# Kernel optimization log

Hardware: AMD Instinct MI355X
Metric: run time of the kernel (lower is better)

Reference implementation:

```python
import jax, jax.numpy as jnp
import numpy as np
from jax import lax

DIM = 1024
EXPAND = 2
D_STATE = 16
D_CONV = 4
DT_RANK = 64  # ceil(DIM/16)
DIM_INNER = DIM * EXPAND
B_SZ, SEQ = 2, 1024


def setup_inputs() -> dict:
    key = jax.random.key(0)
    ks = jax.random.split(key, 8)
    s = lambda fan_in: 1.0 / np.sqrt(fan_in)
    x = jax.random.normal(ks[0], (B_SZ, SEQ, DIM), dtype=jnp.float32)
    W_in = jax.random.normal(ks[1], (DIM, 2 * DIM_INNER), dtype=jnp.float32) * s(DIM)
    conv_w = jax.random.normal(ks[2], (DIM_INNER, D_CONV), dtype=jnp.float32) * s(D_CONV)
    conv_b = jax.random.normal(ks[3], (DIM_INNER,), dtype=jnp.float32) * s(D_CONV)
    W_x = jax.random.normal(ks[4], (DIM_INNER, DT_RANK + 2 * D_STATE), dtype=jnp.float32) * s(DIM_INNER)
    W_dt = jax.random.normal(ks[5], (DT_RANK, DIM_INNER), dtype=jnp.float32) * s(DT_RANK)
    b_dt = jax.random.normal(ks[6], (DIM_INNER,), dtype=jnp.float32) * s(DT_RANK)
    # A_log = log(repeat(arange(1, d_state+1), 'n -> d n'))
    A_log = jnp.broadcast_to(jnp.log(jnp.arange(1, D_STATE + 1, dtype=jnp.float32)), (DIM_INNER, D_STATE))
    D = jnp.ones((DIM_INNER,), dtype=jnp.float32)
    W_out = jax.random.normal(ks[7], (DIM_INNER, DIM), dtype=jnp.float32) * s(DIM_INNER)
    return {"x": x, "W_in": W_in, "conv_w": conv_w, "conv_b": conv_b,
            "W_x": W_x, "W_dt": W_dt, "b_dt": b_dt, "A_log": A_log, "D": D, "W_out": W_out}


def _mamba_forward(x, W_in, conv_w, conv_b, W_x, W_dt, b_dt, A_log, D, W_out):
    b, l, d = x.shape
    di = W_out.shape[0]  # dim_inner
    n = A_log.shape[1]   # d_state
    dt_rank = W_dt.shape[0]

    # in_proj (no bias) and split into ssm branch / gate residual
    x_and_res = x @ W_in                      # [b, l, 2*di]
    u, res = jnp.split(x_and_res, 2, axis=-1)  # each [b, l, di]

    # causal depthwise conv1d along sequence (torch pads both sides then slices [:l])
    pad = conv_w.shape[1] - 1
    up = jnp.pad(u, ((0, 0), (pad, 0), (0, 0)))
    kernel = conv_w.T[:, None, :]  # [W=d_conv, I=1, O=di]
    u = lax.conv_general_dilated(up, kernel, window_strides=(1,), padding='VALID',
                                 dimension_numbers=('NWC', 'WIO', 'NWC'),
                                 feature_group_count=di) + conv_b
    u = jax.nn.silu(u)  # [b, l, di]

    # input-dependent SSM params
    x_dbl = u @ W_x  # [b, l, dt_rank + 2n]
    delta_r, Bm, Cm = jnp.split(x_dbl, [dt_rank, dt_rank + n], axis=-1)
    delta = jax.nn.softplus(delta_r @ W_dt + b_dt)  # [b, l, di]
    A = -jnp.exp(A_log)  # [di, n]

    deltaA = jnp.exp(jnp.einsum('bld,dn->bldn', delta, A))        # [b, l, di, n]
    deltaB_u = jnp.einsum('bld,bln,bld->bldn', delta, Bm, u)       # [b, l, di, n]

    def step(h, inp):
        dA_t, dBu_t, c_t = inp            # [b,di,n], [b,di,n], [b,n]
        h = dA_t * h + dBu_t
        y_t = jnp.einsum('bdn,bn->bd', h, c_t)
        return h, y_t

    h0 = jnp.zeros((b, di, n), dtype=u.dtype)
    xs = (jnp.moveaxis(deltaA, 1, 0), jnp.moveaxis(deltaB_u, 1, 0), jnp.moveaxis(Cm, 1, 0))
    _, ys = lax.scan(step, h0, xs)        # ys: [l, b, di]
    y = jnp.moveaxis(ys, 0, 1)            # [b, l, di]
    y = y + u * D                          # skip term

    y = y * jax.nn.silu(res)               # gate
    return y @ W_out                       # [b, l, dim]


def reference(x, W_in, conv_w, conv_b, W_x, W_dt, b_dt, A_log, D, W_out):
    return _mamba_forward(x, W_in, conv_w, conv_b, W_x, W_dt, b_dt, A_log, D, W_out)
```

## Files before the change

kernel.cpp:

```cpp
#include <hip/hip_runtime.h>
#include <hip/hip_bf16.h>
#include <math.h>


__device__ __forceinline__ float silu_f(float x) {
    return x / (1.f + __expf(-x));
}
__device__ __forceinline__ unsigned short f2bf(float f) {
    __hip_bfloat16 h = __float2bfloat16(f);
    return *(unsigned short*)&h;
}
__device__ __forceinline__ float bf2f(unsigned short u) {
    return __uint_as_float((unsigned)u << 16);
}

typedef __attribute__((ext_vector_type(8))) short short8v;
typedef __attribute__((ext_vector_type(4))) float f32x4;

__device__ __forceinline__ void gload16(const void* g, void* lds) {
    __builtin_amdgcn_global_load_lds(
        (const __attribute__((address_space(1))) unsigned int*)g,
        (__attribute__((address_space(3))) unsigned int*)lds, 16, 0, 0);
}

template<int MODE>
__global__ __launch_bounds__(256) void gemm_bf16(
    const unsigned short* __restrict__ A,
    const unsigned short* __restrict__ BT,
    float* __restrict__ C,
    unsigned short* __restrict__ Cb,
    const float* __restrict__ bias,
    int M, int N, int K, int klen)
{
    __shared__ unsigned short As[128 * 32];
    __shared__ unsigned short Bs[128 * 32];
    const int tid  = threadIdx.x;
    const int wid  = tid >> 6;
    const int lane = tid & 63;
    const int wr = wid >> 1, wc = wid & 1;
    const int row0 = blockIdx.y * 128, col0 = blockIdx.x * 128;
    const int kbeg = blockIdx.z * klen;
    C += (size_t)blockIdx.z * M * N;

    f32x4 acc[4][4] = {};

    const int srow = lane >> 2;
    const int scol = (lane & 3) * 8;

    for (int k0 = kbeg; k0 < kbeg + klen; k0 += 32) {
        #pragma unroll
        for (int c = 0; c < 2; ++c) {
            int chunk = wid * 2 + c;
            gload16(A  + (size_t)(row0 + chunk * 16 + srow) * K + k0 + scol,
                    (void*)(As + chunk * 512));
            gload16(BT + (size_t)(col0 + chunk * 16 + srow) * K + k0 + scol,
                    (void*)(Bs + chunk * 512));
        }
        __syncthreads();
        short8v a[4], b[4];
        #pragma unroll
        for (int i = 0; i < 4; ++i)
            a[i] = *(const short8v*)&As[(wr * 64 + i * 16 + (lane & 15)) * 32 + (lane >> 4) * 8];
        #pragma unroll
        for (int j = 0; j < 4; ++j)
            b[j] = *(const short8v*)&Bs[(wc * 64 + j * 16 + (lane & 15)) * 32 + (lane >> 4) * 8];
        #pragma unroll
        for (int i = 0; i < 4; ++i)
            #pragma unroll
            for (int j = 0; j < 4; ++j)
                acc[i][j] = __builtin_amdgcn_mfma_f32_16x16x32_bf16(a[i], b[j], acc[i][j], 0, 0, 0);
        __syncthreads();
    }

    #pragma unroll
    for (int i = 0; i < 4; ++i) {
        int rbase = row0 + wr * 64 + i * 16 + (lane >> 4) * 4;
        #pragma unroll
        for (int j = 0; j < 4; ++j) {
            int cc = col0 + wc * 64 + j * 16 + (lane & 15);
            float bi = (MODE == 3) ? bias[cc] : 0.f;
            #pragma unroll
            for (int r = 0; r < 4; ++r) {
                float v = acc[i][j][r];
                if (MODE == 3) {
                    v += bi;
                    v = (v > 20.f) ? v : __logf(1.f + __expf(v));
                    Cb[(size_t)(rbase + r) * N + cc] = f2bf(v);
                } else {
                    C[(size_t)(rbase + r) * N + cc] = v;
                }
            }
        }
    }
}

__device__ __forceinline__ void trans64(
    const float* __restrict__ W, unsigned short* __restrict__ WT,
    int K, int N, int bk, int bn, int tid, float (*t)[65])
{
    const int tx = tid & 63, ty = tid >> 6;
    #pragma unroll
    for (int s = 0; s < 16; ++s)
        t[ty + 4 * s][tx] = W[(size_t)(bk + ty + 4 * s) * N + bn + tx];
    __syncthreads();
    #pragma unroll
    for (int s = 0; s < 16; ++s)
        WT[(size_t)(bn + ty + 4 * s) * K + bk + tx] = f2bf(t[tx][ty + 4 * s]);
}

__global__ __launch_bounds__(256) void prep_all(
    const float* __restrict__ x,
    const float* __restrict__ W_in,
    const float* __restrict__ W_out,
    const float* __restrict__ Wx,
    const float* __restrict__ Wdt,
    unsigned short* __restrict__ xb,
    unsigned short* __restrict__ W_inT,
    unsigned short* __restrict__ W_outT,
    unsigned short* __restrict__ W_xTp,
    unsigned short* __restrict__ W_dtTp)
{
    __shared__ float t[64][65];
    const int bid = blockIdx.x;
    const int tid = threadIdx.x;
    if (bid < 1024) {
        int i = bid * 256 + tid;
        float4 v0 = *(const float4*)(x + (size_t)i * 8);
        float4 v1 = *(const float4*)(x + (size_t)i * 8 + 4);
        ushort4 o0, o1;
        o0.x = f2bf(v0.x); o0.y = f2bf(v0.y); o0.z = f2bf(v0.z); o0.w = f2bf(v0.w);
        o1.x = f2bf(v1.x); o1.y = f2bf(v1.y); o1.z = f2bf(v1.z); o1.w = f2bf(v1.w);
        *(ushort4*)(xb + (size_t)i * 8) = o0;
        *(ushort4*)(xb + (size_t)i * 8 + 4) = o1;
    } else if (bid < 2048) {
        int tt = bid - 1024;
        trans64(W_in, W_inT, 1024, 4096, (tt >> 6) * 64, (tt & 63) * 64, tid, t);
    } else if (bid < 2560) {
        int tt = bid - 2048;
        trans64(W_out, W_outT, 2048, 1024, (tt >> 4) * 64, (tt & 15) * 64, tid, t);
    } else if (bid < 3584) {
        int idx = (bid - 2560) * 256 + tid;
        int k = idx & 2047, n = idx >> 11;
        float v = (n < 96) ? Wx[(size_t)k * 96 + n] : 0.f;
        W_xTp[idx] = f2bf(v);
    } else {
        int idx = (bid - 3584) * 256 + tid;
        int k = idx & 127, n = idx >> 7;
        float v = (k < 64) ? Wdt[(size_t)k * 2048 + n] : 0.f;
        W_dtTp[idx] = f2bf(v);
    }
}

__global__ __launch_bounds__(256) void reduce16(
    const float* __restrict__ P, float* __restrict__ dst,
    unsigned short* __restrict__ dstb)
{
    int i = blockIdx.x * 256 + threadIdx.x;
    const float4* P4 = (const float4*)P;
    float4 s = P4[i];
    #pragma unroll
    for (int k = 1; k < 16; ++k) {
        float4 v = P4[i + (size_t)k * 65536];
        s.x += v.x; s.y += v.y; s.z += v.z; s.w += v.w;
    }
    ((float4*)dst)[i] = s;
    ushort4 o;
    o.x = f2bf(s.x); o.y = f2bf(s.y); o.z = f2bf(s.z); o.w = f2bf(s.w);
    ((ushort4*)dstb)[i] = o;
}

__global__ __launch_bounds__(256) void reduce2(
    const float* __restrict__ P, float* __restrict__ dst)
{
    int i = blockIdx.x * 256 + threadIdx.x;
    const float4* P4 = (const float4*)P;
    float4 a = P4[i], b = P4[i + 524288];
    a.x += b.x; a.y += b.y; a.z += b.z; a.w += b.w;
    ((float4*)dst)[i] = a;
}

__global__ __launch_bounds__(256) void conv_silu(
    const float* __restrict__ xr,
    const float* __restrict__ conv_w,
    const float* __restrict__ conv_b,
    unsigned short* __restrict__ ub)
{
    int idx = blockIdx.x * 256 + threadIdx.x;
    int d = idx & 2047;
    int r = idx >> 11;
    int l = r & 1023;
    int b = r >> 10;
    float acc = conv_b[d];
    const float* wp = conv_w + d * 4;
    #pragma unroll
    for (int w = 0; w < 4; ++w) {
        int ls = l + w - 3;
        if (ls >= 0)
            acc = fmaf(xr[((size_t)((b << 10) + ls) << 12) + d], wp[w], acc);
    }
    ub[idx] = f2bf(silu_f(acc));
}

#define SCAN_T 16
#define NSEG 8
#define SEGLEN 128

__device__ __forceinline__ size_t stash_idx(int j) {
    return ((size_t)(j >> 11) << 12) + (j & 2047);
}

#define DPP_ADD(v, ctrl) ((v) + __int_as_float(__builtin_amdgcn_update_dpp( \
        0, __float_as_int(v), (ctrl), 0xF, 0xF, true)))

__global__ __launch_bounds__(256) void scan_pass1(
    const unsigned short* __restrict__ delta_b,
    const unsigned short* __restrict__ ub,
    const float* __restrict__ xdbl,
    const float* __restrict__ A_log,
    float* __restrict__ stash)
{
    __shared__ float2 du[2][SCAN_T][17];
    __shared__ float  bs[2][SCAN_T][17];

    const int tid = threadIdx.x;
    const int dg = blockIdx.x, b = blockIdx.y, s = blockIdx.z;
    const int d0 = dg * 16;
    const int ch = tid >> 4, n = tid & 15;
    const float Aval = -__expf(A_log[(d0 + ch) * 16 + n]);
    const int sli = tid >> 4, sc = tid & 15;
    const int lbase = s * SEGLEN;

    float g_d, g_u, g_b;
    {
        size_t row = (size_t)(b << 10) + lbase + sli;
        g_d = bf2f(delta_b[(row << 11) + d0 + sc]);
        g_u = bf2f(ub[(row << 11) + d0 + sc]);
        g_b = xdbl[(row << 7) + 64 + sc];
    }
    du[0][sli][sc] = make_float2(g_d, g_u);
    bs[0][sli][sc] = g_b;
    __syncthreads();

    float h = 0.f, sd = 0.f;
    int cb = 0;
    for (int c = 0; c < SEGLEN / SCAN_T; ++c) {
        const bool more = (c + 1) < SEGLEN / SCAN_T;
        if (more) {
            size_t row = (size_t)(b << 10) + lbase + (c + 1) * SCAN_T + sli;
            g_d = bf2f(delta_b[(row << 11) + d0 + sc]);
            g_u = bf2f(ub[(row << 11) + d0 + sc]);
            g_b = xdbl[(row << 7) + 64 + sc];
        }
        float e_[SCAN_T], f_[SCAN_T];
        #pragma unroll
        for (int li = 0; li < SCAN_T; ++li) {
            float2 duv = du[cb][li][ch];
            float bv = bs[cb][li][n];
            e_[li] = __expf(duv.x * Aval);
            f_[li] = duv.x * bv * duv.y;
            sd += duv.x;
        }
        #pragma unroll
        for (int li = 0; li < SCAN_T; ++li)
            h = fmaf(e_[li], h, f_[li]);
        if (more) {
            du[cb ^ 1][sli][sc] = make_float2(g_d, g_u);
            bs[cb ^ 1][sli][sc] = g_b;
        }
        __syncthreads();
        cb ^= 1;
    }
    int j = (((b << 3) + s) * 128 + dg) * 256 + tid;
    stash[stash_idx(j)] = __expf(Aval * sd);
    stash[stash_idx(j + 524288)] = h;
}

__global__ __launch_bounds__(256) void scan_pass3(
    const unsigned short* __restrict__ delta_b,
    const unsigned short* __restrict__ ub,
    const float* __restrict__ xdbl,
    const float* __restrict__ A_log,
    const float* __restrict__ xr,
    const float* __restrict__ Dv,
    unsigned short* __restrict__ ysb)
{
    __shared__ float2 du[2][SCAN_T][17];
    __shared__ float2 bc[2][SCAN_T][17];
    __shared__ float  rs[2][SCAN_T][17];

    const int tid = threadIdx.x;
    const int dg = blockIdx.x, b = blockIdx.y, s = blockIdx.z;
    const int d0 = dg * 16;
    const int ch = tid >> 4, n = tid & 15;
    const float Aval = -__expf(A_log[(d0 + ch) * 16 + n]);
    const float Dval = Dv[d0 + ch];
    const int sli = tid >> 4, sc = tid & 15;
    const int lbase = s * SEGLEN;

    float h = 0.f;
    for (int sp = 0; sp < s; ++sp) {
        int j = (((b << 3) + sp) * 128 + dg) * 256 + tid;
        h = fmaf(xr[stash_idx(j)], h, xr[stash_idx(j + 524288)]);
    }

    float g_d, g_u, g_b, g_c, g_r;
    {
        size_t row = (size_t)(b << 10) + lbase + sli;
        g_d = bf2f(delta_b[(row << 11) + d0 + sc]);
        g_u = bf2f(ub[(row << 11) + d0 + sc]);
        g_b = xdbl[(row << 7) + 64 + sc];
        g_c = xdbl[(row << 7) + 80 + sc];
        g_r = xr[(row << 12) + 2048 + d0 + sc];
    }
    du[0][sli][sc] = make_float2(g_d, g_u);
    bc[0][sli][sc] = make_float2(g_b, g_c);
    rs[0][sli][sc] = g_r;
    __syncthreads();

    int cb = 0;
    for (int c = 0; c < SEGLEN / SCAN_T; ++c) {
        const int l0 = lbase + c * SCAN_T;
        const bool more = (c + 1) < SEGLEN / SCAN_T;
        if (more) {
            size_t row = (size_t)(b << 10) + l0 + SCAN_T + sli;
            g_d = bf2f(delta_b[(row << 11) + d0 + sc]);
            g_u = bf2f(ub[(row << 11) + d0 + sc]);
            g_b = xdbl[(row << 7) + 64 + sc];
            g_c = xdbl[(row << 7) + 80 + sc];
            g_r = xr[(row << 12) + 2048 + d0 + sc];
        }
        float e_[SCAN_T], f_[SCAN_T], c_[SCAN_T];
        #pragma unroll
        for (int li = 0; li < SCAN_T; ++li) {
            float2 duv = du[cb][li][ch];
            float2 bcv = bc[cb][li][n];
            e_[li] = __expf(duv.x * Aval);
            f_[li] = duv.x * bcv.x * duv.y;
            c_[li] = bcv.y;
        }
        float mysum = 0.f;
        #pragma unroll
        for (int li = 0; li < SCAN_T; ++li) {
            h = fmaf(e_[li], h, f_[li]);
            float pv = h * c_[li];
            pv = DPP_ADD(pv, 0xB1);
            pv = DPP_ADD(pv, 0x4E);
            pv = DPP_ADD(pv, 0x141);
            pv = DPP_ADD(pv, 0x140);
            mysum = (n == li) ? pv : mysum;
        }
        {
            float2 duv = du[cb][n][ch];
            float resv = rs[cb][n][ch];
            float outv = (mysum + duv.y * Dval) * silu_f(resv);
            ysb[((size_t)((b << 10) + l0 + n) << 11) + d0 + ch] = f2bf(outv);
        }
        if (more) {
            du[cb ^ 1][sli][sc] = make_float2(g_d, g_u);
            bc[cb ^ 1][sli][sc] = make_float2(g_b, g_c);
            rs[cb ^ 1][sli][sc] = g_r;
        }
        __syncthreads();
        cb ^= 1;
    }
}

extern "C" void kernel_launch(void* const* d_in, const int* in_sizes, int n_in,
                              void* d_out, int out_size, void* d_ws, size_t ws_size,
                              hipStream_t stream)
{
    const float* x      = (const float*)d_in[0];
    const float* W_in   = (const float*)d_in[1];
    const float* conv_w = (const float*)d_in[2];
    const float* conv_b = (const float*)d_in[3];
    const float* W_x    = (const float*)d_in[4];
    const float* W_dt   = (const float*)d_in[5];
    const float* b_dt   = (const float*)d_in[6];
    const float* A_log  = (const float*)d_in[7];
    const float* Dv     = (const float*)d_in[8];
    const float* W_out  = (const float*)d_in[9];
    float* out = (float*)d_out;

    float* ws    = (float*)d_ws;
    float* xr    = ws;
    float* xdbl  = ws + (size_t)8388608;
    float* P16   = ws + (size_t)8650752;
    float* P2    = ws + (size_t)12845056;
    unsigned short* bfr = (unsigned short*)(ws + (size_t)17039360);
    unsigned short* xb      = bfr;
    unsigned short* W_inT   = bfr + (size_t)2097152;
    unsigned short* W_xTp   = bfr + (size_t)6291456;
    unsigned short* W_dtTp  = bfr + (size_t)6553600;
    unsigned short* W_outT  = bfr + (size_t)6815744;
    unsigned short* ub      = bfr + (size_t)8912896;
    unsigned short* delta_b = bfr + (size_t)13107200;
    unsigned short* ysb     = bfr + (size_t)17301504;
    unsigned short* xdbl_b  = bfr + (size_t)21495808;

    prep_all<<<4608, 256, 0, stream>>>(x, W_in, W_out, W_x, W_dt,
                                       xb, W_inT, W_outT, W_xTp, W_dtTp);
    gemm_bf16<0><<<dim3(32, 16, 1), 256, 0, stream>>>(xb, W_inT, xr, nullptr, nullptr, 2048, 4096, 1024, 1024);
    conv_silu<<<16384, 256, 0, stream>>>(xr, conv_w, conv_b, ub);
    gemm_bf16<0><<<dim3(1, 16, 16), 256, 0, stream>>>(ub, W_xTp, P16, nullptr, nullptr, 2048, 128, 2048, 128);
    reduce16<<<256, 256, 0, stream>>>(P16, xdbl, xdbl_b);
    gemm_bf16<3><<<dim3(16, 16, 1), 256, 0, stream>>>(xdbl_b, W_dtTp, nullptr, delta_b, b_dt, 2048, 2048, 128, 128);
    scan_pass1<<<dim3(128, 2, 8), 256, 0, stream>>>(delta_b, ub, xdbl, A_log, xr);
    scan_pass3<<<dim3(128, 2, 8), 256, 0, stream>>>(delta_b, ub, xdbl, A_log, xr, Dv, ysb);
    gemm_bf16<0><<<dim3(8, 16, 2), 256, 0, stream>>>(ysb, W_outT, P2, nullptr, nullptr, 2048, 1024, 2048, 1024);
    reduce2<<<2048, 256, 0, stream>>>(P2, out);
}
```

Baseline: 168.4 us.

## Store in_proj output as bf16, fuse weight prep into GEMM1, widen split-K

The in_proj GEMM now writes its output in bf16 with paired 32-bit stores, and conv_silu and scan_pass3 read that bf16 buffer, cutting memory traffic on the largest intermediate. The W_out/W_x/W_dt weight conversions move into the same launch as the in_proj GEMM so they overlap with it, and the W_x/W_dt conversions are vectorised four elements at a time. conv_silu processes four channels per thread. The scan stash gets its own buffer, and the out_proj split-K goes from 2 to 4 with a 4-way reduce. Rounding the residual/gate branch to bf16 adds some precision loss.

```diff
diff --git a/kernel.cpp b/kernel.cpp
--- a/kernel.cpp
+++ b/kernel.cpp
@@ -21,6 +21,79 @@
     __builtin_amdgcn_global_load_lds(
         (const __attribute__((address_space(1))) unsigned int*)g,
         (__attribute__((address_space(3))) unsigned int*)lds, 16, 0, 0);
+}
+
+template<int MODE>
+__device__ __forceinline__ void gemm_core(
+    const unsigned short* __restrict__ A,
+    const unsigned short* __restrict__ BT,
+    float* __restrict__ C, unsigned short* __restrict__ Cb,
+    const float* __restrict__ bias,
+    int M, int N, int K, int kbeg, int klen,
+    int bx, int by, unsigned short* As, unsigned short* Bs)
+{
+    const int tid  = threadIdx.x;
+    const int wid  = tid >> 6;
+    const int lane = tid & 63;
+    const int wr = wid >> 1, wc = wid & 1;
+    const int row0 = by * 128, col0 = bx * 128;
+
+    f32x4 acc[4][4] = {};
+
+    const int srow = lane >> 2;
+    const int scol = (lane & 3) * 8;
+
+    for (int k0 = kbeg; k0 < kbeg + klen; k0 += 32) {
+        #pragma unroll
+        for (int c = 0; c < 2; ++c) {
+            int chunk = wid * 2 + c;
+            gload16(A  + (size_t)(row0 + chunk * 16 + srow) * K + k0 + scol,
+                    (void*)(As + chunk * 512));
+            gload16(BT + (size_t)(col0 + chunk * 16 + srow) * K + k0 + scol,
+                    (void*)(Bs + chunk * 512));
+        }
+        __syncthreads();
+        short8v a[4], b[4];
+        #pragma unroll
+        for (int i = 0; i < 4; ++i)
+            a[i] = *(const short8v*)&As[(wr * 64 + i * 16 + (lane & 15)) * 32 + (lane >> 4) * 8];
+        #pragma unroll
+        for (int j = 0; j < 4; ++j)
+            b[j] = *(const short8v*)&Bs[(wc * 64 + j * 16 + (lane & 15)) * 32 + (lane >> 4) * 8];
+        #pragma unroll
+        for (int i = 0; i < 4; ++i)
+            #pragma unroll
+            for (int j = 0; j < 4; ++j)
+                acc[i][j] = __builtin_amdgcn_mfma_f32_16x16x32_bf16(a[i], b[j], acc[i][j], 0, 0, 0);
+        __syncthreads();
+    }
+
+    #pragma unroll
+    for (int i = 0; i < 4; ++i) {
+        int rbase = row0 + wr * 64 + i * 16 + (lane >> 4) * 4;
+        #pragma unroll
+        for (int j = 0; j < 4; ++j) {
+            int cc = col0 + wc * 64 + j * 16 + (lane & 15);
+            float bi = (MODE == 3) ? bias[cc] : 0.f;
+            #pragma unroll
+            for (int r = 0; r < 4; ++r) {
+                float v = acc[i][j][r];
+                if (MODE == 0) {
+                    C[(size_t)(rbase + r) * N + cc] = v;
+                } else {
+                    if (MODE == 3) {
+                        v += bi;
+                        v = (v > 20.f) ? v : __logf(1.f + __expf(v));
+                    }
+                    unsigned short m = f2bf(v);
+                    unsigned other = (unsigned)__shfl_xor((int)m, 1, 64) & 0xffffu;
+                    if (!(lane & 1))
+                        *(unsigned*)(Cb + (size_t)(rbase + r) * N + cc) =
+                            (unsigned)m | (other << 16);
+                }
+            }
+        }
+    }
 }
 
 template<int MODE>
@@ -34,64 +107,9 @@
 {
     __shared__ unsigned short As[128 * 32];
     __shared__ unsigned short Bs[128 * 32];
-    const int tid  = threadIdx.x;
-    const int wid  = tid >> 6;
-    const int lane = tid & 63;
-    const int wr = wid >> 1, wc = wid & 1;
-    const int row0 = blockIdx.y * 128, col0 = blockIdx.x * 128;
-    const int kbeg = blockIdx.z * klen;
-    C += (size_t)blockIdx.z * M * N;
-
-    f32x4 acc[4][4] = {};
-
-    const int srow = lane >> 2;
-    const int scol = (lane & 3) * 8;
-
-    for (int k0 = kbeg; k0 < kbeg + klen; k0 += 32) {
-        #pragma unroll
-        for (int c = 0; c < 2; ++c) {
-            int chunk = wid * 2 + c;
-            gload16(A  + (size_t)(row0 + chunk * 16 + srow) * K + k0 + scol,
-                    (void*)(As + chunk * 512));
-            gload16(BT + (size_t)(col0 + chunk * 16 + srow) * K + k0 + scol,
-                    (void*)(Bs + chunk * 512));
-        }
-        __syncthreads();
-        short8v a[4], b[4];
-        #pragma unroll
-        for (int i = 0; i < 4; ++i)
-            a[i] = *(const short8v*)&As[(wr * 64 + i * 16 + (lane & 15)) * 32 + (lane >> 4) * 8];
-        #pragma unroll
-        for (int j = 0; j < 4; ++j)
-            b[j] = *(const short8v*)&Bs[(wc * 64 + j * 16 + (lane & 15)) * 32 + (lane >> 4) * 8];
-        #pragma unroll
-        for (int i = 0; i < 4; ++i)
-            #pragma unroll
-            for (int j = 0; j < 4; ++j)
-                acc[i][j] = __builtin_amdgcn_mfma_f32_16x16x32_bf16(a[i], b[j], acc[i][j], 0, 0, 0);
-        __syncthreads();
-    }
-
-    #pragma unroll
-    for (int i = 0; i < 4; ++i) {
-        int rbase = row0 + wr * 64 + i * 16 + (lane >> 4) * 4;
-        #pragma unroll
-        for (int j = 0; j < 4; ++j) {
-            int cc = col0 + wc * 64 + j * 16 + (lane & 15);
-            float bi = (MODE == 3) ? bias[cc] : 0.f;
-            #pragma unroll
-            for (int r = 0; r < 4; ++r) {
-                float v = acc[i][j][r];
-                if (MODE == 3) {
-                    v += bi;
-                    v = (v > 20.f) ? v : __logf(1.f + __expf(v));
-                    Cb[(size_t)(rbase + r) * N + cc] = f2bf(v);
-                } else {
-                    C[(size_t)(rbase + r) * N + cc] = v;
-                }
-            }
-        }
-    }
+    gemm_core<MODE>(A, BT, C + (size_t)blockIdx.z * M * N, Cb, bias,
+                    M, N, K, blockIdx.z * klen, klen,
+                    blockIdx.x, blockIdx.y, As, Bs);
 }
 
 __device__ __forceinline__ void trans64(
@@ -108,17 +126,55 @@
         WT[(size_t)(bn + ty + 4 * s) * K + bk + tx] = f2bf(t[tx][ty + 4 * s]);
 }
 
-__global__ __launch_bounds__(256) void prep_all(
-    const float* __restrict__ x,
-    const float* __restrict__ W_in,
+__global__ __launch_bounds__(256) void gemm1_fused(
+    const unsigned short* __restrict__ xb,
+    const unsigned short* __restrict__ W_inT,
+    unsigned short* __restrict__ xrb,
     const float* __restrict__ W_out,
     const float* __restrict__ Wx,
     const float* __restrict__ Wdt,
-    unsigned short* __restrict__ xb,
-    unsigned short* __restrict__ W_inT,
     unsigned short* __restrict__ W_outT,
     unsigned short* __restrict__ W_xTp,
     unsigned short* __restrict__ W_dtTp)
+{
+    __shared__ char smem[64 * 65 * 4];
+    const int bid = blockIdx.x;
+    const int tid = threadIdx.x;
+    if (bid < 512) {
+        unsigned short* As = (unsigned short*)smem;
+        unsigned short* Bs = As + 128 * 32;
+        gemm_core<4>(xb, W_inT, nullptr, xrb, nullptr,
+                     2048, 4096, 1024, 0, 1024, bid & 31, bid >> 5, As, Bs);
+    } else if (bid < 1024) {
+        int tt = bid - 512;
+        trans64(W_out, W_outT, 2048, 1024, (tt >> 4) * 64, (tt & 15) * 64,
+                tid, (float(*)[65])smem);
+    } else if (bid < 1280) {
+        int idx4 = (bid - 1024) * 256 + tid;
+        int n = idx4 >> 9, k0 = (idx4 & 511) << 2;
+        ushort4 o;
+        o.x = f2bf((n < 96) ? Wx[(size_t)(k0 + 0) * 96 + n] : 0.f);
+        o.y = f2bf((n < 96) ? Wx[(size_t)(k0 + 1) * 96 + n] : 0.f);
+        o.z = f2bf((n < 96) ? Wx[(size_t)(k0 + 2) * 96 + n] : 0.f);
+        o.w = f2bf((n < 96) ? Wx[(size_t)(k0 + 3) * 96 + n] : 0.f);
+        *(ushort4*)(W_xTp + (size_t)idx4 * 4) = o;
+    } else {
+        int idx4 = (bid - 1280) * 256 + tid;
+        int n = idx4 >> 5, k0 = (idx4 & 31) << 2;
+        ushort4 o;
+        o.x = f2bf((k0 + 0 < 64) ? Wdt[(size_t)(k0 + 0) * 2048 + n] : 0.f);
+        o.y = f2bf((k0 + 1 < 64) ? Wdt[(size_t)(k0 + 1) * 2048 + n] : 0.f);
+        o.z = f2bf((k0 + 2 < 64) ? Wdt[(size_t)(k0 + 2) * 2048 + n] : 0.f);
+        o.w = f2bf((k0 + 3 < 64) ? Wdt[(size_t)(k0 + 3) * 2048 + n] : 0.f);
+        *(ushort4*)(W_dtTp + (size_t)idx4 * 4) = o;
+    }
+}
+
+__global__ __launch_bounds__(256) void prep(
+    const float* __restrict__ x,
+    const float* __restrict__ W_in,
+    unsigned short* __restrict__ xb,
+    unsigned short* __restrict__ W_inT)
 {
     __shared__ float t[64][65];
     const int bid = blockIdx.x;
@@ -132,22 +188,9 @@
         o1.x = f2bf(v1.x); o1.y = f2bf(v1.y); o1.z = f2bf(v1.z); o1.w = f2bf(v1.w);
         *(ushort4*)(xb + (size_t)i * 8) = o0;
         *(ushort4*)(xb + (size_t)i * 8 + 4) = o1;
-    } else if (bid < 2048) {
+    } else {
         int tt = bid - 1024;
         trans64(W_in, W_inT, 1024, 4096, (tt >> 6) * 64, (tt & 63) * 64, tid, t);
-    } else if (bid < 2560) {
-        int tt = bid - 2048;
-        trans64(W_out, W_outT, 2048, 1024, (tt >> 4) * 64, (tt & 15) * 64, tid, t);
-    } else if (bid < 3584) {
-        int idx = (bid - 2560) * 256 + tid;
-        int k = idx & 2047, n = idx >> 11;
-        float v = (n < 96) ? Wx[(size_t)k * 96 + n] : 0.f;
-        W_xTp[idx] = f2bf(v);
-    } else {
-        int idx = (bid - 3584) * 256 + tid;
-        int k = idx & 127, n = idx >> 7;
-        float v = (k < 64) ? Wdt[(size_t)k * 2048 + n] : 0.f;
-        W_dtTp[idx] = f2bf(v);
     }
 }
 
@@ -169,45 +212,62 @@
     ((ushort4*)dstb)[i] = o;
 }
 
-__global__ __launch_bounds__(256) void reduce2(
+__global__ __launch_bounds__(256) void reduce4(
     const float* __restrict__ P, float* __restrict__ dst)
 {
     int i = blockIdx.x * 256 + threadIdx.x;
     const float4* P4 = (const float4*)P;
-    float4 a = P4[i], b = P4[i + 524288];
-    a.x += b.x; a.y += b.y; a.z += b.z; a.w += b.w;
-    ((float4*)dst)[i] = a;
+    float4 s = P4[i];
+    #pragma unroll
+    for (int k = 1; k < 4; ++k) {
+        float4 v = P4[i + (size_t)k * 524288];
+        s.x += v.x; s.y += v.y; s.z += v.z; s.w += v.w;
+    }
+    ((float4*)dst)[i] = s;
 }
 
 __global__ __launch_bounds__(256) void conv_silu(
-    const float* __restrict__ xr,
+    const unsigned short* __restrict__ xrb,
     const float* __restrict__ conv_w,
     const float* __restrict__ conv_b,
     unsigned short* __restrict__ ub)
 {
-    int idx = blockIdx.x * 256 + threadIdx.x;
-    int d = idx & 2047;
-    int r = idx >> 11;
-    int l = r & 1023;
-    int b = r >> 10;
-    float acc = conv_b[d];
-    const float* wp = conv_w + d * 4;
+    int t = blockIdx.x * 256 + threadIdx.x;
+    int d4 = (t & 511) << 2;
+    int r = t >> 9;
+    int l = r & 1023, b = r >> 10;
+    float4 cb4 = *(const float4*)(conv_b + d4);
+    float acc[4] = {cb4.x, cb4.y, cb4.z, cb4.w};
+    float4 cw0 = *(const float4*)(conv_w + (size_t)(d4 + 0) * 4);
+    float4 cw1 = *(const float4*)(conv_w + (size_t)(d4 + 1) * 4);
+    float4 cw2 = *(const float4*)(conv_w + (size_t)(d4 + 2) * 4);
+    float4 cw3 = *(const float4*)(conv_w + (size_t)(d4 + 3) * 4);
+    float w0a[4] = {cw0.x, cw0.y, cw0.z, cw0.w};
+    float w1a[4] = {cw1.x, cw1.y, cw1.z, cw1.w};
+    float w2a[4] = {cw2.x, cw2.y, cw2.z, cw2.w};
+    float w3a[4] = {cw3.x, cw3.y, cw3.z, cw3.w};
     #pragma unroll
     for (int w = 0; w < 4; ++w) {
         int ls = l + w - 3;
-        if (ls >= 0)
-            acc = fmaf(xr[((size_t)((b << 10) + ls) << 12) + d], wp[w], acc);
-    }
-    ub[idx] = f2bf(silu_f(acc));
+        if (ls >= 0) {
+            ushort4 xv = *(const ushort4*)(xrb + (((size_t)((b << 10) + ls)) << 12) + d4);
+            acc[0] = fmaf(bf2f(xv.x), w0a[w], acc[0]);
+            acc[1] = fmaf(bf2f(xv.y), w1a[w], acc[1]);
+            acc[2] = fmaf(bf2f(xv.z), w2a[w], acc[2]);
+            acc[3] = fmaf(bf2f(xv.w), w3a[w], acc[3]);
+        }
+    }
+    ushort4 o;
+    o.x = f2bf(silu_f(acc[0]));
+    o.y = f2bf(silu_f(acc[1]));
+    o.z = f2bf(silu_f(acc[2]));
+    o.w = f2bf(silu_f(acc[3]));
+    *(ushort4*)(ub + (size_t)t * 4) = o;
 }
 
 #define SCAN_T 16
 #define NSEG 8
 #define SEGLEN 128
-
-__device__ __forceinline__ size_t stash_idx(int j) {
-    return ((size_t)(j >> 11) << 12) + (j & 2047);
-}
 
 #define DPP_ADD(v, ctrl) ((v) + __int_as_float(__builtin_amdgcn_update_dpp( \
         0, __float_as_int(v), (ctrl), 0xF, 0xF, true)))
@@ -271,8 +331,8 @@
         cb ^= 1;
     }
     int j = (((b << 3) + s) * 128 + dg) * 256 + tid;
-    stash[stash_idx(j)] = __expf(Aval * sd);
-    stash[stash_idx(j + 524288)] = h;
+    stash[j] = __expf(Aval * sd);
+    stash[j + 524288] = h;
 }
 
 __global__ __launch_bounds__(256) void scan_pass3(
@@ -280,7 +340,8 @@
     const unsigned short* __restrict__ ub,
     const float* __restrict__ xdbl,
     const float* __restrict__ A_log,
-    const float* __restrict__ xr,
+    const unsigned short* __restrict__ xrb,
+    const float* __restrict__ stash,
     const float* __restrict__ Dv,
     unsigned short* __restrict__ ysb)
 {
@@ -300,7 +361,7 @@
     float h = 0.f;
     for (int sp = 0; sp < s; ++sp) {
         int j = (((b << 3) + sp) * 128 + dg) * 256 + tid;
-        h = fmaf(xr[stash_idx(j)], h, xr[stash_idx(j + 524288)]);
+        h = fmaf(stash[j], h, stash[j + 524288]);
     }
 
     float g_d, g_u, g_b, g_c, g_r;
@@ -310,7 +371,7 @@
         g_u = bf2f(ub[(row << 11) + d0 + sc]);
         g_b = xdbl[(row << 7) + 64 + sc];
         g_c = xdbl[(row << 7) + 80 + sc];
-        g_r = xr[(row << 12) + 2048 + d0 + sc];
+        g_r = bf2f(xrb[(row << 12) + 2048 + d0 + sc]);
     }
     du[0][sli][sc] = make_float2(g_d, g_u);
     bc[0][sli][sc] = make_float2(g_b, g_c);
@@ -327,7 +388,7 @@
             g_u = bf2f(ub[(row << 11) + d0 + sc]);
             g_b = xdbl[(row << 7) + 64 + sc];
             g_c = xdbl[(row << 7) + 80 + sc];
-            g_r = xr[(row << 12) + 2048 + d0 + sc];
+            g_r = bf2f(xrb[(row << 12) + 2048 + d0 + sc]);
         }
         float e_[SCAN_T], f_[SCAN_T], c_[SCAN_T];
         #pragma unroll
@@ -382,30 +443,31 @@
     float* out = (float*)d_out;
 
     float* ws    = (float*)d_ws;
-    float* xr    = ws;
-    float* xdbl  = ws + (size_t)8388608;
-    float* P16   = ws + (size_t)8650752;
-    float* P2    = ws + (size_t)12845056;
-    unsigned short* bfr = (unsigned short*)(ws + (size_t)17039360);
+    float* xdbl  = ws;
+    float* P16   = ws + (size_t)262144;
+    float* P4    = ws + (size_t)4456448;
+    float* stash = ws + (size_t)12845056;
+    unsigned short* bfr = (unsigned short*)(ws + (size_t)13893632);
     unsigned short* xb      = bfr;
     unsigned short* W_inT   = bfr + (size_t)2097152;
     unsigned short* W_xTp   = bfr + (size_t)6291456;
     unsigned short* W_dtTp  = bfr + (size_t)6553600;
     unsigned short* W_outT  = bfr + (size_t)6815744;
-    unsigned short* ub      = bfr + (size_t)8912896;
-    unsigned short* delta_b = bfr + (size_t)13107200;
-    unsigned short* ysb     = bfr + (size_t)17301504;
-    unsigned short* xdbl_b  = bfr + (size_t)21495808;
-
-    prep_all<<<4608, 256, 0, stream>>>(x, W_in, W_out, W_x, W_dt,
-                                       xb, W_inT, W_outT, W_xTp, W_dtTp);
-    gemm_bf16<0><<<dim3(32, 16, 1), 256, 0, stream>>>(xb, W_inT, xr, nullptr, nullptr, 2048, 4096, 1024, 1024);
-    conv_silu<<<16384, 256, 0, stream>>>(xr, conv_w, conv_b, ub);
+    unsigned short* xrb     = bfr + (size_t)8912896;
+    unsigned short* ub      = bfr + (size_t)17301504;
+    unsigned short* delta_b = bfr + (size_t)21495808;
+    unsigned short* ysb     = bfr + (size_t)25690112;
+    unsigned short* xdbl_b  = bfr + (size_t)29884416;
+
+    prep<<<2048, 256, 0, stream>>>(x, W_in, xb, W_inT);
+    gemm1_fused<<<1536, 256, 0, stream>>>(xb, W_inT, xrb, W_out, W_x, W_dt,
+                                          W_outT, W_xTp, W_dtTp);
+    conv_silu<<<4096, 256, 0, stream>>>(xrb, conv_w, conv_b, ub);
     gemm_bf16<0><<<dim3(1, 16, 16), 256, 0, stream>>>(ub, W_xTp, P16, nullptr, nullptr, 2048, 128, 2048, 128);
     reduce16<<<256, 256, 0, stream>>>(P16, xdbl, xdbl_b);
     gemm_bf16<3><<<dim3(16, 16, 1), 256, 0, stream>>>(xdbl_b, W_dtTp, nullptr, delta_b, b_dt, 2048, 2048, 128, 128);
-    scan_pass1<<<dim3(128, 2, 8), 256, 0, stream>>>(delta_b, ub, xdbl, A_log, xr);
-    scan_pass3<<<dim3(128, 2, 8), 256, 0, stream>>>(delta_b, ub, xdbl, A_log, xr, Dv, ysb);
-    gemm_bf16<0><<<dim3(8, 16, 2), 256, 0, stream>>>(ysb, W_outT, P2, nullptr, nullptr, 2048, 1024, 2048, 1024);
-    reduce2<<<2048, 256, 0, stream>>>(P2, out);
-}
+    scan_pass1<<<dim3(128, 2, 8), 256, 0, stream>>>(delta_b, ub, xdbl, A_log, stash);
+    scan_pass3<<<dim3(128, 2, 8), 256, 0, stream>>>(delta_b, ub, xdbl, A_log, xrb, stash, Dv, ysb);
+    gemm_bf16<0><<<dim3(8, 16, 4), 256, 0, stream>>>(ysb, W_outT, P4, nullptr, nullptr, 2048, 1024, 2048, 512);
+    reduce4<<<2048, 256, 0, stream>>>(P4, out);
+}
```

Result: faster. 155.7 us (-7.5%).
